# Performance work log

Measured on AMD Instinct MI355X. Metric: run time of the kernel, lower is better.

The kernel has to match this reference:

```python
import jax, jax.numpy as jnp
import numpy as np

N_SAMPLES = 32768
ATOM_LEN = 8192
N_ATOMS = 16
MODEL_DIM = 128
GRID = 128  # n_freqs == n_frames == 128
LOWEST_FREQ = 30.0 / 11025.0  # 30 Hz / nyquist of 22050 Hz


def conv2d(x, w, b, stride=1, pad=1):
    y = jax.lax.conv_general_dilated(x, w, (stride, stride), [(pad, pad), (pad, pad)],
                                     dimension_numbers=('NCHW', 'OIHW', 'NCHW'))
    return y + b[None, :, None, None]


def conv1d(x, w, b, pad=1):
    y = jax.lax.conv_general_dilated(x, w, (1,), [(pad, pad)],
                                     dimension_numbers=('NCH', 'OIH', 'NCH'))
    return y + b[None, :, None]


def lrelu(x):
    return jnp.where(x >= 0, x, 0.2 * x)


def up2d(x):
    return jnp.repeat(jnp.repeat(x, 2, axis=2), 2, axis=3)


def _forward(x, pos, wi, bi, wp, bp, ws1, bs1, ws2, bs2, ws3, bs3, ws4, bs4,
             wsb, bsb, wsel, bsel, wval, bval, wup, bup, wu1, bu1, wu2, bu2,
             wu3, bu3, wamp, bamp, wfr, bfr, wnz, bnz, noise):
    B = x.shape[0]
    h = conv2d(x, wi, bi)                                   # [B,112,128,128]
    p = jnp.broadcast_to(pos[None], (B,) + pos.shape)
    h = jnp.concatenate([h, p], axis=1)                     # [B,128,128,128]
    h = conv2d(h, wp, bp)
    # sparse trunk: /2, /2, x2, x2 back to 128x128
    h = lrelu(conv2d(h, ws1, bs1, stride=2))                # 64x64
    h = lrelu(conv2d(h, ws2, bs2, stride=2))                # 32x32
    h = up2d(h)
    h = lrelu(conv2d(h, ws3, bs3))                          # 64x64
    h = up2d(h)
    h = lrelu(conv2d(h, ws4, bs4))                          # 128x128
    # SparseBlock
    h = conv2d(h, wsb, bsb)
    norms = jnp.sqrt(jnp.sum(h * h, axis=1, keepdims=True))
    normed = h / (norms + 1e-8)
    s = conv2d(normed, wsel, bsel, pad=0)                   # [B,1,128,128]
    s = jax.nn.softmax(s.reshape(B, GRID * GRID), axis=-1)
    _, indices = jax.lax.top_k(s, N_ATOMS)                  # [B,16]
    values = conv2d(h, wval, bval, pad=0)                   # [B,128,128,128]
    f = indices // GRID
    t = indices % GRID
    # gather latents; the original multiplies by val + (1-val) == 1
    latents = values[jnp.arange(B)[:, None], :, f, t]       # [B,16,128]
    feat_map = s.reshape(B, GRID, GRID)
    # --- AudioModel on flattened atoms ---
    z = latents.reshape(B * N_ATOMS, MODEL_DIM)
    u = (z @ wup + bup).reshape(-1, MODEL_DIM, 4)           # ConvUpsample start: [N,128,4]
    for w, bb in ((wu1, bu1), (wu2, bu2), (wu3, bu3)):      # 4->8->16->32 frames
        u = jnp.repeat(u, 2, axis=2)
        u = lrelu(conv1d(u, w, bb))
    # oscillator bank: amp = params**2, freq constrained to [lowest, 1]
    amp = conv1d(u, wamp, bamp, pad=0) ** 2                 # [N,128,32]
    fr = jax.nn.sigmoid(conv1d(u, wfr, bfr, pad=0))
    fr = LOWEST_FREQ + fr * (1.0 - LOWEST_FREQ)
    amp = jnp.repeat(amp, ATOM_LEN // 32, axis=2)           # [N,128,8192]
    fr = jnp.repeat(fr, ATOM_LEN // 32, axis=2)
    phase = jnp.cumsum(fr * jnp.pi, axis=2)
    harm = jnp.sum(jnp.sin(phase) * amp, axis=1)            # [N,8192]
    # noise model: per-frame rfft magnitudes (squared) applied to white noise frames
    mags = conv1d(u, wnz, bnz, pad=0) ** 2                  # [N,129,32]
    spec = jnp.fft.rfft(noise, axis=-1)                     # [N,32,129]
    filt = spec * jnp.transpose(mags, (0, 2, 1))
    nz = jnp.fft.irfft(filt, n=256, axis=-1).reshape(-1, ATOM_LEN).astype(harm.dtype)
    atoms = (harm + nz).reshape(B, N_ATOMS, ATOM_LEN)
    # --- batched dynamic-offset scatter-add ---
    L = N_SAMPLES + ATOM_LEN
    offs = indices[:, :, None] + jnp.arange(ATOM_LEN)[None, None, :]  # [B,16,8192]
    out = jnp.zeros((B, L), atoms.dtype).at[jnp.arange(B)[:, None, None], offs].add(atoms)
    output = out[:, :N_SAMPLES][:, None, :]
    return output, latents, feat_map


def setup_inputs() -> dict:
    key = jax.random.key(0)
    ks = jax.random.split(key, 40)
    r = lambda i, shape, s=0.05: jax.random.normal(ks[i], shape, dtype=jnp.float32) * s
    B = 2
    d = {}
    d['x'] = jax.random.normal(ks[0], (B, 1, GRID, GRID), dtype=jnp.float32)
    pos = r(1, (16, GRID, GRID), 1.0)
    d['pos'] = pos / (jnp.sqrt(jnp.sum(pos * pos, axis=0, keepdims=True)) + 1e-8)
    d['wi'] = r(2, (112, 1, 3, 3)); d['bi'] = jnp.zeros(112, jnp.float32)
    d['wp'] = r(3, (128, 128, 3, 3)); d['bp'] = jnp.zeros(128, jnp.float32)
    d['ws1'] = r(4, (128, 128, 3, 3)); d['bs1'] = jnp.zeros(128, jnp.float32)
    d['ws2'] = r(5, (128, 128, 3, 3)); d['bs2'] = jnp.zeros(128, jnp.float32)
    d['ws3'] = r(6, (128, 128, 3, 3)); d['bs3'] = jnp.zeros(128, jnp.float32)
    d['ws4'] = r(7, (128, 128, 3, 3)); d['bs4'] = jnp.zeros(128, jnp.float32)
    d['wsb'] = r(8, (128, 128, 3, 3)); d['bsb'] = jnp.zeros(128, jnp.float32)
    d['wsel'] = r(9, (1, 128, 1, 1)); d['bsel'] = jnp.zeros(1, jnp.float32)
    d['wval'] = r(10, (128, 128, 1, 1)); d['bval'] = jnp.zeros(128, jnp.float32)
    d['wup'] = r(11, (128, 512)); d['bup'] = jnp.zeros(512, jnp.float32)
    d['wu1'] = r(12, (128, 128, 3)); d['bu1'] = jnp.zeros(128, jnp.float32)
    d['wu2'] = r(13, (128, 128, 3)); d['bu2'] = jnp.zeros(128, jnp.float32)
    d['wu3'] = r(14, (128, 128, 3)); d['bu3'] = jnp.zeros(128, jnp.float32)
    d['wamp'] = r(15, (128, 128, 1)); d['bamp'] = jnp.zeros(128, jnp.float32)
    d['wfr'] = r(16, (128, 128, 1)); d['bfr'] = jnp.zeros(128, jnp.float32)
    d['wnz'] = r(17, (129, 128, 1)); d['bnz'] = jnp.zeros(129, jnp.float32)
    d['noise'] = jax.random.normal(ks[18], (B * N_ATOMS, 32, 256), dtype=jnp.float32)
    return d


def reference(x, pos, wi, bi, wp, bp, ws1, bs1, ws2, bs2, ws3, bs3, ws4, bs4,
              wsb, bsb, wsel, bsel, wval, bval, wup, bup, wu1, bu1, wu2, bu2,
              wu3, bu3, wamp, bamp, wfr, bfr, wnz, bnz, noise):
    return _forward(x, pos, wi, bi, wp, bp, ws1, bs1, ws2, bs2, ws3, bs3, ws4, bs4,
                    wsb, bsb, wsel, bsel, wval, bval, wup, bup, wu1, bu1, wu2, bu2,
                    wu3, bu3, wamp, bamp, wfr, bfr, wnz, bnz, noise)
```

## Files before the change

### kernel.cpp

```cpp
#include <hip/hip_runtime.h>
#include <hip/hip_bf16.h>
#include <math.h>

#define LOWEST_FREQ (30.0f / 11025.0f)

typedef _Float16 f16x8 __attribute__((ext_vector_type(8)));
typedef _Float16 f16x4 __attribute__((ext_vector_type(4)));
typedef float f32x4 __attribute__((ext_vector_type(4)));

__device__ __forceinline__ float fast_sin_rev(float rev) {
#if __has_builtin(__builtin_amdgcn_sinf)
    return __builtin_amdgcn_sinf(rev);
#else
    return __sinf(rev * 6.28318530717958647692f);
#endif
}
__device__ __forceinline__ float fast_cos_rev(float rev) {
#if __has_builtin(__builtin_amdgcn_cosf)
    return __builtin_amdgcn_cosf(rev);
#else
    return __cosf(rev * 6.28318530717958647692f);
#endif
}
__device__ __forceinline__ float lrelu(float x) { return x >= 0.f ? x : 0.2f * x; }

__global__ __launch_bounds__(256) void repack_kernel(
    const float* __restrict__ w0, const float* __restrict__ w1,
    const float* __restrict__ w2, const float* __restrict__ w3,
    const float* __restrict__ w4, const float* __restrict__ w5,
    _Float16* __restrict__ whi, _Float16* __restrict__ wlo)
{
    int idx = blockIdx.x * 256 + threadIdx.x;
    if (idx >= 6 * 147456) return;
    int j   = idx / 147456;
    int rem = idx - j * 147456;
    int tap = rem >> 14;
    int oc  = (rem >> 7) & 127;
    int ic  = rem & 127;
    const float* src = (j == 0) ? w0 : (j == 1) ? w1 : (j == 2) ? w2 :
                       (j == 3) ? w3 : (j == 4) ? w4 : w5;
    float v = src[(oc * 128 + ic) * 9 + tap];
    _Float16 h = (_Float16)v;
    whi[idx] = h;
    wlo[idx] = (_Float16)(v - (float)h);
}

__global__ __launch_bounds__(256) void conv_in_kernel(
    const float* __restrict__ x, const float* __restrict__ wi,
    const float* __restrict__ bi, const float* __restrict__ pos,
    _Float16* __restrict__ outHi, _Float16* __restrict__ outLo, int total)
{
    int idx = blockIdx.x * 256 + threadIdx.x;
    if (idx >= total) return;
    int c   = idx & 127;
    int pix = (idx >> 7) & 16383;
    int b   = idx >> 21;
    int y = pix >> 7, xx = pix & 127;
    float v;
    if (c < 112) {
        float acc = bi[c];
        const float* xb = x + (size_t)b * 16384;
        const float* wc = wi + c * 9;
        #pragma unroll
        for (int ky = 0; ky < 3; ++ky) {
            int gy = y + ky - 1;
            if ((unsigned)gy < 128u) {
                #pragma unroll
                for (int kx = 0; kx < 3; ++kx) {
                    int gx = xx + kx - 1;
                    if ((unsigned)gx < 128u)
                        acc = fmaf(wc[ky * 3 + kx], xb[gy * 128 + gx], acc);
                }
            }
        }
        v = acc;
    } else {
        v = pos[(c - 112) * 16384 + pix];
    }
    _Float16 h = (_Float16)v;
    outHi[idx] = h;
    outLo[idx] = (_Float16)(v - (float)h);
}

template<bool UP2, bool RELU, bool SPLITOUT>
__global__ __launch_bounds__(256, 2) void mfma_conv_s1(
    const _Float16* __restrict__ inHi, const _Float16* __restrict__ inLo,
    const _Float16* __restrict__ whi, const _Float16* __restrict__ wlo,
    const float* __restrict__ bias, float* __restrict__ outF,
    _Float16* __restrict__ outHi, _Float16* __restrict__ outLo,
    int H, int W)
{
    __shared__ __align__(16) _Float16 sAh[10 * 18 * 72];
    __shared__ __align__(16) _Float16 sAl[10 * 18 * 72];
    const int tid  = threadIdx.x;
    const int w    = tid >> 6, lane = tid & 63;
    const int wm   = w & 1, wn = w >> 1;
    const int lm   = lane & 15, lq = lane >> 4;
    const int b    = blockIdx.z >> 1;
    const int ocb  = (blockIdx.z & 1) * 64;
    const int x0   = blockIdx.x * 16, y0 = blockIdx.y * 8;
    const int iy0  = y0 - 1, ix0 = x0 - 1;
    const int Hp   = UP2 ? (H >> 1) : H;
    const int Wp   = UP2 ? (W >> 1) : W;
    const _Float16* inbH = inHi + (size_t)b * Hp * Wp * 128;
    const _Float16* inbL = inLo + (size_t)b * Hp * Wp * 128;
    const f16x4 zf4 = {(_Float16)0.f, (_Float16)0.f, (_Float16)0.f, (_Float16)0.f};

    f16x4 rh[12], rl[12];

#define S1_PREF(ICS)                                                          \
    _Pragma("unroll")                                                         \
    for (int i = 0; i < 12; ++i) {                                            \
        int e = tid + i * 256;                                                \
        rh[i] = zf4; rl[i] = zf4;                                             \
        if (e < 2880) {                                                       \
            int px = e >> 4, icq = e & 15;                                    \
            int row = px / 18, col = px - row * 18;                           \
            int gy = iy0 + row, gx = ix0 + col;                               \
            if ((unsigned)gy < (unsigned)H && (unsigned)gx < (unsigned)W) {   \
                int sy = UP2 ? (gy >> 1) : gy;                                \
                int sx = UP2 ? (gx >> 1) : gx;                                \
                size_t o = ((size_t)sy * Wp + sx) * 128 + (ICS) + icq * 4;    \
                rh[i] = *(const f16x4*)(inbH + o);                            \
                rl[i] = *(const f16x4*)(inbL + o);                            \
            }                                                                 \
        }                                                                     \
    }

#define S1_WRITE()                                                            \
    _Pragma("unroll")                                                         \
    for (int i = 0; i < 12; ++i) {                                            \
        int e = tid + i * 256;                                                \
        if (e < 2880) {                                                       \
            int px = e >> 4, icq = e & 15;                                    \
            *(f16x4*)&sAh[px * 72 + icq * 4] = rh[i];                         \
            *(f16x4*)&sAl[px * 72 + icq * 4] = rl[i];                         \
        }                                                                     \
    }

    f32x4 acc[4][2];
    #pragma unroll
    for (int r = 0; r < 4; ++r)
        #pragma unroll
        for (int nt = 0; nt < 2; ++nt) acc[r][nt] = (f32x4){0.f, 0.f, 0.f, 0.f};

    S1_PREF(0)
    S1_WRITE()
    __syncthreads();

    for (int ics2 = 0; ics2 < 2; ++ics2) {
        const int ics = ics2 * 64;
        if (ics2 == 0) { S1_PREF(64) }

        for (int ky = 0; ky < 3; ++ky)
        for (int kx = 0; kx < 3; ++kx) {
            const int tap = ky * 3 + kx;
            const _Float16* wth = whi + (size_t)tap * 16384;
            const _Float16* wtl = wlo + (size_t)tap * 16384;
            #pragma unroll
            for (int kc = 0; kc < 2; ++kc) {
                f16x8 bh[2], bl[2];
                #pragma unroll
                for (int nt = 0; nt < 2; ++nt) {
                    int oc = ocb + wn * 32 + nt * 16 + lm;
                    size_t o = (size_t)oc * 128 + ics + kc * 32 + lq * 8;
                    bh[nt] = *(const f16x8*)(wth + o);
                    bl[nt] = *(const f16x8*)(wtl + o);
                }
                #pragma unroll
                for (int r = 0; r < 4; ++r) {
                    int rin = wm * 4 + r + ky;
                    int cin = lm + kx;
                    int o = (rin * 18 + cin) * 72 + kc * 32 + lq * 8;
                    f16x8 ah = *(const f16x8*)(&sAh[o]);
                    f16x8 al = *(const f16x8*)(&sAl[o]);
                    #pragma unroll
                    for (int nt = 0; nt < 2; ++nt) {
                        acc[r][nt] = __builtin_amdgcn_mfma_f32_16x16x32_f16(ah, bh[nt], acc[r][nt], 0, 0, 0);
                        acc[r][nt] = __builtin_amdgcn_mfma_f32_16x16x32_f16(ah, bl[nt], acc[r][nt], 0, 0, 0);
                        acc[r][nt] = __builtin_amdgcn_mfma_f32_16x16x32_f16(al, bh[nt], acc[r][nt], 0, 0, 0);
                    }
                }
            }
        }
        __syncthreads();
        if (ics2 == 0) { S1_WRITE() __syncthreads(); }
    }
#undef S1_PREF
#undef S1_WRITE

    float bv[2];
    #pragma unroll
    for (int nt = 0; nt < 2; ++nt) bv[nt] = bias[ocb + wn * 32 + nt * 16 + lm];
    const size_t boff = (size_t)b * H * W * 128;
    #pragma unroll
    for (int r = 0; r < 4; ++r) {
        int y = y0 + wm * 4 + r;
        #pragma unroll
        for (int nt = 0; nt < 2; ++nt) {
            int oc = ocb + wn * 32 + nt * 16 + lm;
            #pragma unroll
            for (int reg = 0; reg < 4; ++reg) {
                int xo = x0 + lq * 4 + reg;
                float vv = acc[r][nt][reg] + bv[nt];
                if (RELU) vv = lrelu(vv);
                size_t oo = boff + ((size_t)y * W + xo) * 128 + oc;
                if (SPLITOUT) {
                    _Float16 hh = (_Float16)vv;
                    outHi[oo] = hh;
                    outLo[oo] = (_Float16)(vv - (float)hh);
                } else {
                    outF[oo] = vv;
                }
            }
        }
    }
}

template<bool RELU, bool SPLITOUT>
__global__ __launch_bounds__(256, 2) void mfma_conv_s2(
    const _Float16* __restrict__ inHi, const _Float16* __restrict__ inLo,
    const _Float16* __restrict__ whi, const _Float16* __restrict__ wlo,
    const float* __restrict__ bias, float* __restrict__ outF,
    _Float16* __restrict__ outHi, _Float16* __restrict__ outLo,
    int Hin, int Win)
{
    __shared__ __align__(16) _Float16 sAh[9 * 33 * 40];
    __shared__ __align__(16) _Float16 sAl[9 * 33 * 40];
    const int tid  = threadIdx.x;
    const int w    = tid >> 6, lane = tid & 63;
    const int lm   = lane & 15, lq = lane >> 4;
    const int wn   = w;
    const int b    = blockIdx.z;
    const int Wout = Win >> 1;
    const int x0   = blockIdx.x * 16, y0 = blockIdx.y * 4;
    const int iy0  = blockIdx.y * 8 - 1, ix0 = blockIdx.x * 32 - 1;
    const _Float16* inbH = inHi + (size_t)b * Hin * Win * 128;
    const _Float16* inbL = inLo + (size_t)b * Hin * Win * 128;
    const f16x4 zf4 = {(_Float16)0.f, (_Float16)0.f, (_Float16)0.f, (_Float16)0.f};

    f16x4 rh[10], rl[10];

#define S2_PREF(ICS)                                                          \
    _Pragma("unroll")                                                         \
    for (int i = 0; i < 10; ++i) {                                            \
        int e = tid + i * 256;                                                \
        rh[i] = zf4; rl[i] = zf4;                                             \
        if (e < 2376) {                                                       \
            int px = e >> 3, icq = e & 7;                                     \
            int row = px / 33, col = px - row * 33;                           \
            int gy = iy0 + row, gx = ix0 + col;                               \
            if ((unsigned)gy < (unsigned)Hin && (unsigned)gx < (unsigned)Win) { \
                size_t o = ((size_t)gy * Win + gx) * 128 + (ICS) + icq * 4;   \
                rh[i] = *(const f16x4*)(inbH + o);                            \
                rl[i] = *(const f16x4*)(inbL + o);                            \
            }                                                                 \
        }                                                                     \
    }

#define S2_WRITE()                                                            \
    _Pragma("unroll")                                                         \
    for (int i = 0; i < 10; ++i) {                                            \
        int e = tid + i * 256;                                                \
        if (e < 2376) {                                                       \
            int px = e >> 3, icq = e & 7;                                     \
            *(f16x4*)&sAh[px * 40 + icq * 4] = rh[i];                         \
            *(f16x4*)&sAl[px * 40 + icq * 4] = rl[i];                         \
        }                                                                     \
    }

    f32x4 acc[4][2];
    #pragma unroll
    for (int r = 0; r < 4; ++r)
        #pragma unroll
        for (int nt = 0; nt < 2; ++nt) acc[r][nt] = (f32x4){0.f, 0.f, 0.f, 0.f};

    S2_PREF(0)
    S2_WRITE()
    __syncthreads();

    for (int kc = 0; kc < 4; ++kc) {
        if (kc < 3) { S2_PREF((kc + 1) * 32) }

        for (int ky = 0; ky < 3; ++ky)
        for (int kx = 0; kx < 3; ++kx) {
            const int tap = ky * 3 + kx;
            const _Float16* wth = whi + (size_t)tap * 16384;
            const _Float16* wtl = wlo + (size_t)tap * 16384;
            f16x8 bh[2], bl[2];
            #pragma unroll
            for (int nt = 0; nt < 2; ++nt) {
                int oc = wn * 32 + nt * 16 + lm;
                size_t o = (size_t)oc * 128 + kc * 32 + lq * 8;
                bh[nt] = *(const f16x8*)(wth + o);
                bl[nt] = *(const f16x8*)(wtl + o);
            }
            #pragma unroll
            for (int r = 0; r < 4; ++r) {
                int rin = 2 * r + ky;
                int cin = 2 * lm + kx;
                int o = (rin * 33 + cin) * 40 + lq * 8;
                f16x8 ah = *(const f16x8*)(&sAh[o]);
                f16x8 al = *(const f16x8*)(&sAl[o]);
                #pragma unroll
                for (int nt = 0; nt < 2; ++nt) {
                    acc[r][nt] = __builtin_amdgcn_mfma_f32_16x16x32_f16(ah, bh[nt], acc[r][nt], 0, 0, 0);
                    acc[r][nt] = __builtin_amdgcn_mfma_f32_16x16x32_f16(ah, bl[nt], acc[r][nt], 0, 0, 0);
                    acc[r][nt] = __builtin_amdgcn_mfma_f32_16x16x32_f16(al, bh[nt], acc[r][nt], 0, 0, 0);
                }
            }
        }
        __syncthreads();
        if (kc < 3) { S2_WRITE() __syncthreads(); }
    }
#undef S2_PREF
#undef S2_WRITE

    float bv[2];
    #pragma unroll
    for (int nt = 0; nt < 2; ++nt) bv[nt] = bias[wn * 32 + nt * 16 + lm];
    const int Hout = Hin >> 1;
    const size_t boff = (size_t)b * Hout * Wout * 128;
    #pragma unroll
    for (int r = 0; r < 4; ++r) {
        int y = y0 + r;
        #pragma unroll
        for (int nt = 0; nt < 2; ++nt) {
            int oc = wn * 32 + nt * 16 + lm;
            #pragma unroll
            for (int reg = 0; reg < 4; ++reg) {
                int xo = x0 + lq * 4 + reg;
                float vv = acc[r][nt][reg] + bv[nt];
                if (RELU) vv = lrelu(vv);
                size_t oo = boff + ((size_t)y * Wout + xo) * 128 + oc;
                if (SPLITOUT) {
                    _Float16 hh = (_Float16)vv;
                    outHi[oo] = hh;
                    outLo[oo] = (_Float16)(vv - (float)hh);
                } else {
                    outF[oo] = vv;
                }
            }
        }
    }
}

__global__ __launch_bounds__(256) void normsel_kernel(
    const float* __restrict__ h, const float* __restrict__ wsel,
    const float* __restrict__ bsel, float* __restrict__ s_lin, int totalPix)
{
    int wid = (blockIdx.x * 256 + threadIdx.x) >> 6;
    if (wid >= totalPix) return;
    int lane = threadIdx.x & 63;
    const float* hb = h + (size_t)wid * 128;
    float v1 = hb[lane], v2 = hb[lane + 64];
    float ss  = v1 * v1 + v2 * v2;
    float dot = wsel[lane] * v1 + wsel[lane + 64] * v2;
    #pragma unroll
    for (int off = 32; off > 0; off >>= 1) {
        ss  += __shfl_down(ss, off);
        dot += __shfl_down(dot, off);
    }
    if (lane == 0) s_lin[wid] = dot / (sqrtf(ss) + 1e-8f) + bsel[0];
}

__global__ __launch_bounds__(256) void softmax_kernel(
    const float* __restrict__ s_lin, float* __restrict__ feat)
{
    int b = blockIdx.x;
    const float* src = s_lin + b * 16384;
    __shared__ float red[256];
    int tid = threadIdx.x;
    float m = -INFINITY;
    for (int i = tid; i < 16384; i += 256) m = fmaxf(m, src[i]);
    red[tid] = m;
    __syncthreads();
    for (int off = 128; off > 0; off >>= 1) {
        if (tid < off) red[tid] = fmaxf(red[tid], red[tid + off]);
        __syncthreads();
    }
    m = red[0];
    __syncthreads();
    float s = 0.f;
    for (int i = tid; i < 16384; i += 256) s += expf(src[i] - m);
    red[tid] = s;
    __syncthreads();
    for (int off = 128; off > 0; off >>= 1) {
        if (tid < off) red[tid] += red[tid + off];
        __syncthreads();
    }
    s = red[0];
    float inv = 1.f / s;
    for (int i = tid; i < 16384; i += 256) feat[b * 16384 + i] = expf(src[i] - m) * inv;
}

__global__ __launch_bounds__(256) void topk_stage1(
    const float* __restrict__ s_lin, float* __restrict__ cand_v,
    int* __restrict__ cand_i)
{
    __shared__ float sv[256];
    int b = blockIdx.y;
    int chunk = blockIdx.x;
    int tid = threadIdx.x;
    int gidx = chunk * 256 + tid;
    float v = s_lin[b * 16384 + gidx];
    sv[tid] = v;
    __syncthreads();
    int cnt = 0;
    #pragma unroll 8
    for (int j = 0; j < 256; ++j) {
        float vj = sv[j];
        cnt += (vj > v || (vj == v && j < tid)) ? 1 : 0;
    }
    if (cnt < 16) {
        int slot = (b * 64 + chunk) * 16 + cnt;
        cand_v[slot] = v;
        cand_i[slot] = gidx;
    }
}

__global__ __launch_bounds__(1024) void topk_stage2(
    const float* __restrict__ cand_v, const int* __restrict__ cand_i,
    int* __restrict__ idxOut)
{
    __shared__ float sv[1024];
    __shared__ int   si[1024];
    int b = blockIdx.x;
    int tid = threadIdx.x;
    float v  = cand_v[b * 1024 + tid];
    int  idx = cand_i[b * 1024 + tid];
    sv[tid] = v;
    si[tid] = idx;
    __syncthreads();
    int cnt = 0;
    #pragma unroll 8
    for (int j = 0; j < 1024; ++j) {
        float vj = sv[j];
        int  ij = si[j];
        cnt += (vj > v || (vj == v && ij < idx)) ? 1 : 0;
    }
    if (cnt < 16) idxOut[b * 16 + cnt] = idx & 16383;
}

__global__ __launch_bounds__(128) void latents_kernel(
    const float* __restrict__ h, const float* __restrict__ wval,
    const float* __restrict__ bval, const int* __restrict__ tki,
    float* __restrict__ outL, float* __restrict__ zbuf)
{
    int bk = blockIdx.x;
    int oc = threadIdx.x;
    int b = bk >> 4;
    int pix = tki[bk] & 16383;
    const float* hb = h + ((size_t)b * 16384 + pix) * 128;
    const float* wr = wval + oc * 128;
    float acc = bval[oc];
    #pragma unroll 8
    for (int ic = 0; ic < 128; ++ic) acc = fmaf(wr[ic], hb[ic], acc);
    outL[bk * 128 + oc] = acc;
    zbuf[bk * 128 + oc] = acc;
}

__global__ __launch_bounds__(256) void upproj_kernel(
    const float* __restrict__ zbuf, const float* __restrict__ wup,
    const float* __restrict__ bup, float* __restrict__ u0, int total)
{
    int idx = blockIdx.x * 256 + threadIdx.x;
    if (idx >= total) return;
    int a = idx >> 9, o = idx & 511;
    const float* z = zbuf + a * 128;
    float acc = bup[o];
    #pragma unroll 8
    for (int k = 0; k < 128; ++k) acc = fmaf(z[k], wup[k * 512 + o], acc);
    u0[idx] = acc;
}

template<int LIN>
__global__ __launch_bounds__(256) void conv1dup_kernel(
    const float* __restrict__ in, const float* __restrict__ w,
    const float* __restrict__ bias, float* __restrict__ out, int total)
{
    constexpr int LOUT = 2 * LIN;
    constexpr int SH = (LIN == 4) ? 3 : (LIN == 8) ? 4 : 5;
    int idx = blockIdx.x * 256 + threadIdx.x;
    if (idx >= total) return;
    int t  = idx & (LOUT - 1);
    int oc = (idx >> SH) & 127;
    int a  = idx >> (SH + 7);
    float acc = bias[oc];
    const float* ib = in + (size_t)a * 128 * LIN;
    const float* wr = w + (size_t)oc * 384;
    int im_ = (t - 1) >> 1, i0 = t >> 1, ip = (t + 1) >> 1;
    bool bm = (t - 1) >= 0, bp = (t + 1) < LOUT;
    #pragma unroll 4
    for (int ic = 0; ic < 128; ++ic) {
        const float* ii = ib + ic * LIN;
        const float* ww = wr + ic * 3;
        if (bm) acc = fmaf(ww[0], ii[im_], acc);
        acc = fmaf(ww[1], ii[i0], acc);
        if (bp) acc = fmaf(ww[2], ii[ip], acc);
    }
    out[idx] = lrelu(acc);
}

__global__ __launch_bounds__(256) void heads_kernel(
    const float* __restrict__ u,
    const float* __restrict__ wamp, const float* __restrict__ bamp,
    const float* __restrict__ wfr,  const float* __restrict__ bfr,
    const float* __restrict__ wnz,  const float* __restrict__ bnz,
    float* __restrict__ amp, float* __restrict__ fr, float* __restrict__ mags,
    int total)
{
    int idx = blockIdx.x * 256 + threadIdx.x;
    if (idx >= total) return;
    int t  = idx & 31;
    int oc = (idx >> 5) % 385;
    int a  = idx / (32 * 385);
    const float* ib = u + (size_t)a * 4096 + t;
    const float* wr; float bv;
    if (oc < 128)      { wr = wamp + oc * 128;        bv = bamp[oc]; }
    else if (oc < 256) { wr = wfr + (oc - 128) * 128; bv = bfr[oc - 128]; }
    else               { wr = wnz + (oc - 256) * 128; bv = bnz[oc - 256]; }
    float acc = bv;
    #pragma unroll 8
    for (int ic = 0; ic < 128; ++ic) acc = fmaf(wr[ic], ib[ic * 32], acc);
    if (oc < 128) {
        amp[((size_t)a * 128 + oc) * 32 + t] = acc * acc;
    } else if (oc < 256) {
        float s = 1.f / (1.f + expf(-acc));
        fr[((size_t)a * 128 + (oc - 128)) * 32 + t] = LOWEST_FREQ + s * (1.f - LOWEST_FREQ);
    } else {
        mags[((size_t)a * 129 + (oc - 256)) * 32 + t] = acc * acc;
    }
}

__global__ __launch_bounds__(256) void prefix_kernel(
    const float* __restrict__ fr, float* __restrict__ pb, int total)
{
    int i = blockIdx.x * 256 + threadIdx.x;
    if (i >= total) return;
    const float* f = fr + i * 32;
    float* p = pb + i * 32;
    double s = 0.0;
    for (int j = 0; j < 32; ++j) {
        double t = 128.0 * s;
        p[j] = (float)(t - floor(t));
        s += (double)f[j];
    }
}

__global__ __launch_bounds__(256) void harm_kernel(
    const float* __restrict__ fr, const float* __restrict__ amp,
    const float* __restrict__ pb, const int* __restrict__ tki,
    float* __restrict__ outp, int total)
{
    int idx = blockIdx.x * 256 + threadIdx.x;
    if (idx >= total) return;
    int a = idx >> 13;
    int i = idx & 8191;
    int j = i >> 8;
    float il1 = (float)((i & 255) + 1);
    int base = a * 4096 + j;
    float acc = 0.f;
    #pragma unroll 4
    for (int c = 0; c < 128; ++c) {
        int o = base + c * 32;
        float f = fr[o];
        float am = amp[o];
        float p = pb[o];
        float rev = fmaf(il1, 0.5f * f, p);
        acc = fmaf(fast_sin_rev(rev), am, acc);
    }
    int b = a >> 4;
    atomicAdd(outp + (size_t)b * 32768 + (tki[a] & 16383) + i, acc);
}

__global__ __launch_bounds__(256) void spec_kernel(
    const float* __restrict__ noise, float* __restrict__ re,
    float* __restrict__ im, int total)
{
    int idx = blockIdx.x * 256 + threadIdx.x;
    if (idx >= total) return;
    int f  = idx % 129;
    int aw = idx / 129;
    const float* np_ = noise + (size_t)aw * 256;
    float sr = 0.f, si = 0.f;
    for (int n = 0; n < 256; ++n) {
        float rev = (float)(f * n) * (1.0f / 256.0f);
        float c = fast_cos_rev(rev);
        float s = fast_sin_rev(rev);
        float v = np_[n];
        sr = fmaf(v, c, sr);
        si = fmaf(v, -s, si);
    }
    re[idx] = sr;
    im[idx] = si;
}

__global__ __launch_bounds__(256) void nz_kernel(
    const float* __restrict__ re, const float* __restrict__ im,
    const float* __restrict__ mags, const int* __restrict__ tki,
    float* __restrict__ outp, int total)
{
    int idx = blockIdx.x * 256 + threadIdx.x;
    if (idx >= total) return;
    int t  = idx & 255;
    int w_ = (idx >> 8) & 31;
    int a  = idx >> 13;
    const float* R = re + ((size_t)a * 32 + w_) * 129;
    const float* I = im + ((size_t)a * 32 + w_) * 129;
    const float* M = mags + (size_t)a * 129 * 32 + w_;
    float acc = R[0] * M[0];
    #pragma unroll 4
    for (int f = 1; f < 128; ++f) {
        float rev = (float)(f * t) * (1.0f / 256.0f);
        float c = fast_cos_rev(rev);
        float s = fast_sin_rev(rev);
        acc = fmaf(2.f * M[f * 32], fmaf(R[f], c, -I[f] * s), acc);
    }
    float sg = (t & 1) ? -1.f : 1.f;
    acc = fmaf(M[128 * 32] * sg, R[128], acc);
    acc *= (1.f / 256.f);
    int b = a >> 4;
    atomicAdd(outp + (size_t)b * 32768 + (tki[a] & 16383) + (w_ << 8) + t, acc);
}

extern "C" void kernel_launch(void* const* d_in, const int* in_sizes, int n_in,
                              void* d_out, int out_size, void* d_ws, size_t ws_size,
                              hipStream_t stream) {
    (void)n_in; (void)ws_size;
    const float* x    = (const float*)d_in[0];
    const float* pos  = (const float*)d_in[1];
    const float* wi   = (const float*)d_in[2];
    const float* bi   = (const float*)d_in[3];
    const float* wp   = (const float*)d_in[4];
    const float* bp   = (const float*)d_in[5];
    const float* ws1  = (const float*)d_in[6];
    const float* bs1  = (const float*)d_in[7];
    const float* ws2  = (const float*)d_in[8];
    const float* bs2  = (const float*)d_in[9];
    const float* ws3  = (const float*)d_in[10];
    const float* bs3  = (const float*)d_in[11];
    const float* ws4  = (const float*)d_in[12];
    const float* bs4  = (const float*)d_in[13];
    const float* wsb  = (const float*)d_in[14];
    const float* bsb  = (const float*)d_in[15];
    const float* wsel = (const float*)d_in[16];
    const float* bsel = (const float*)d_in[17];
    const float* wval = (const float*)d_in[18];
    const float* bval = (const float*)d_in[19];
    const float* wup  = (const float*)d_in[20];
    const float* bup  = (const float*)d_in[21];
    const float* wu1  = (const float*)d_in[22];
    const float* bu1  = (const float*)d_in[23];
    const float* wu2  = (const float*)d_in[24];
    const float* bu2  = (const float*)d_in[25];
    const float* wu3  = (const float*)d_in[26];
    const float* bu3  = (const float*)d_in[27];
    const float* wamp = (const float*)d_in[28];
    const float* bamp = (const float*)d_in[29];
    const float* wfr  = (const float*)d_in[30];
    const float* bfr  = (const float*)d_in[31];
    const float* wnz  = (const float*)d_in[32];
    const float* bnz  = (const float*)d_in[33];
    const float* noise= (const float*)d_in[34];

    const int B = in_sizes[0] / (128 * 128);
    float* outp = (float*)d_out;
    float* outL = outp + (size_t)B * 32768;
    float* feat = outL + (size_t)B * 16 * 128;

    const size_t BIGF = (size_t)B * 16384 * 128;
    float* hbA = (float*)d_ws;
    float* hbB = hbA + BIGF;
    _Float16* Ahi = (_Float16*)hbA;  _Float16* Alo = Ahi + BIGF;
    _Float16* Bhi = (_Float16*)hbB;  _Float16* Blo = Bhi + BIGF;
    _Float16* whi = (_Float16*)(hbB + BIGF);
    _Float16* wlo = whi + 6 * 147456;
    float* s_lin = (float*)(wlo + 6 * 147456);
    float* tscr  = s_lin + (size_t)B * 16384;
    int*   tki   = (int*)(tscr + (size_t)B * 16384);
    float* zbuf  = (float*)(tki + 64);
    float* u0    = zbuf + (size_t)B * 2048;
    float* u1    = u0 + (size_t)B * 65536;
    float* ampb  = u1 + (size_t)B * 65536;
    float* frb   = ampb + (size_t)B * 65536;
    float* pbb   = frb + (size_t)B * 65536;
    float* magsb = pbb + (size_t)B * 65536;
    float* spR   = magsb + (size_t)B * 16 * 129 * 32;
    float* spI   = spR + (size_t)B * 16 * 32 * 129;

    float* cand_v = tscr;
    int*   cand_i = (int*)(tscr + (size_t)B * 1024);

    hipMemsetAsync(d_out, 0, (size_t)out_size * sizeof(float), stream);

    repack_kernel<<<(6 * 147456 + 255) / 256, 256, 0, stream>>>(wp, ws1, ws2, ws3, ws4, wsb, whi, wlo);

    {
        int total = B * 128 * 16384;
        conv_in_kernel<<<(total + 255) / 256, 256, 0, stream>>>(x, wi, bi, pos, Ahi, Alo, total);
    }
    mfma_conv_s1<false, false, true ><<<dim3(8, 16, B * 2), 256, 0, stream>>>(Ahi, Alo, whi + 0 * 147456, wlo + 0 * 147456, bp,  nullptr, Bhi, Blo, 128, 128);
    mfma_conv_s2<true,  true        ><<<dim3(4, 16, B),     256, 0, stream>>>(Bhi, Blo, whi + 1 * 147456, wlo + 1 * 147456, bs1, nullptr, Ahi, Alo, 128, 128);
    mfma_conv_s2<true,  true        ><<<dim3(2, 8,  B),     256, 0, stream>>>(Ahi, Alo, whi + 2 * 147456, wlo + 2 * 147456, bs2, nullptr, Bhi, Blo, 64, 64);
    mfma_conv_s1<true,  true,  true ><<<dim3(4, 8,  B * 2), 256, 0, stream>>>(Bhi, Blo, whi + 3 * 147456, wlo + 3 * 147456, bs3, nullptr, Ahi, Alo, 64, 64);
    mfma_conv_s1<true,  true,  true ><<<dim3(8, 16, B * 2), 256, 0, stream>>>(Ahi, Alo, whi + 4 * 147456, wlo + 4 * 147456, bs4, nullptr, Bhi, Blo, 128, 128);
    mfma_conv_s1<false, false, false><<<dim3(8, 16, B * 2), 256, 0, stream>>>(Bhi, Blo, whi + 5 * 147456, wlo + 5 * 147456, bsb, hbA,    nullptr, nullptr, 128, 128);
    float* h = hbA;

    {
        int totalPix = B * 16384;
        normsel_kernel<<<(totalPix * 64 + 255) / 256, 256, 0, stream>>>(h, wsel, bsel, s_lin, totalPix);
    }
    softmax_kernel<<<B, 256, 0, stream>>>(s_lin, feat);
    topk_stage1<<<dim3(64, B), 256, 0, stream>>>(s_lin, cand_v, cand_i);
    topk_stage2<<<B, 1024, 0, stream>>>(cand_v, cand_i, tki);
    latents_kernel<<<B * 16, 128, 0, stream>>>(h, wval, bval, tki, outL, zbuf);

    {
        int total = B * 16 * 512;
        upproj_kernel<<<(total + 255) / 256, 256, 0, stream>>>(zbuf, wup, bup, u0, total);
    }
    {
        int total = B * 16 * 128 * 8;
        conv1dup_kernel<4><<<(total + 255) / 256, 256, 0, stream>>>(u0, wu1, bu1, u1, total);
    }
    {
        int total = B * 16 * 128 * 16;
        conv1dup_kernel<8><<<(total + 255) / 256, 256, 0, stream>>>(u1, wu2, bu2, u0, total);
    }
    {
        int total = B * 16 * 128 * 32;
        conv1dup_kernel<16><<<(total + 255) / 256, 256, 0, stream>>>(u0, wu3, bu3, u1, total);
    }
    {
        int total = B * 16 * 385 * 32;
        heads_kernel<<<(total + 255) / 256, 256, 0, stream>>>(u1, wamp, bamp, wfr, bfr, wnz, bnz,
                                                              ampb, frb, magsb, total);
    }
    {
        int total = B * 16 * 128;
        prefix_kernel<<<(total + 255) / 256, 256, 0, stream>>>(frb, pbb, total);
    }
    {
        int total = B * 16 * 8192;
        harm_kernel<<<(total + 255) / 256, 256, 0, stream>>>(frb, ampb, pbb, tki, outp, total);
    }
    {
        int total = B * 16 * 32 * 129;
        spec_kernel<<<(total + 255) / 256, 256, 0, stream>>>(noise, spR, spI, total);
    }
    {
        int total = B * 16 * 32 * 256;
        nz_kernel<<<(total + 255) / 256, 256, 0, stream>>>(spR, spI, magsb, tki, outp, total);
    }
}
```

Before: 650.7 us.

## Fuse audio decoder stages into one kernel and parallelize softmax using topk max

```diff
diff --git a/kernel.cpp b/kernel.cpp
--- a/kernel.cpp
+++ b/kernel.cpp
@@ -364,36 +364,6 @@
     if (lane == 0) s_lin[wid] = dot / (sqrtf(ss) + 1e-8f) + bsel[0];
 }
 
-__global__ __launch_bounds__(256) void softmax_kernel(
-    const float* __restrict__ s_lin, float* __restrict__ feat)
-{
-    int b = blockIdx.x;
-    const float* src = s_lin + b * 16384;
-    __shared__ float red[256];
-    int tid = threadIdx.x;
-    float m = -INFINITY;
-    for (int i = tid; i < 16384; i += 256) m = fmaxf(m, src[i]);
-    red[tid] = m;
-    __syncthreads();
-    for (int off = 128; off > 0; off >>= 1) {
-        if (tid < off) red[tid] = fmaxf(red[tid], red[tid + off]);
-        __syncthreads();
-    }
-    m = red[0];
-    __syncthreads();
-    float s = 0.f;
-    for (int i = tid; i < 16384; i += 256) s += expf(src[i] - m);
-    red[tid] = s;
-    __syncthreads();
-    for (int off = 128; off > 0; off >>= 1) {
-        if (tid < off) red[tid] += red[tid + off];
-        __syncthreads();
-    }
-    s = red[0];
-    float inv = 1.f / s;
-    for (int i = tid; i < 16384; i += 256) feat[b * 16384 + i] = expf(src[i] - m) * inv;
-}
-
 __global__ __launch_bounds__(256) void topk_stage1(
     const float* __restrict__ s_lin, float* __restrict__ cand_v,
     int* __restrict__ cand_i)
@@ -421,7 +391,7 @@
 
 __global__ __launch_bounds__(1024) void topk_stage2(
     const float* __restrict__ cand_v, const int* __restrict__ cand_i,
-    int* __restrict__ idxOut)
+    int* __restrict__ idxOut, float* __restrict__ maxOut)
 {
     __shared__ float sv[1024];
     __shared__ int   si[1024];
@@ -439,7 +409,37 @@
         int  ij = si[j];
         cnt += (vj > v || (vj == v && ij < idx)) ? 1 : 0;
     }
-    if (cnt < 16) idxOut[b * 16 + cnt] = idx & 16383;
+    if (cnt < 16) {
+        idxOut[b * 16 + cnt] = idx & 16383;
+        if (cnt == 0) maxOut[b] = v;
+    }
+}
+
+__global__ __launch_bounds__(256) void softmax_sum_kernel(
+    const float* __restrict__ s_lin, const float* __restrict__ maxv,
+    float* __restrict__ denom)
+{
+    __shared__ float red[4];
+    int b = blockIdx.y;
+    int i = blockIdx.x * 256 + threadIdx.x;
+    float m = maxv[b];
+    float e = expf(s_lin[b * 16384 + i] - m);
+    #pragma unroll
+    for (int off = 32; off > 0; off >>= 1) e += __shfl_down(e, off);
+    int lane = threadIdx.x & 63, wv = threadIdx.x >> 6;
+    if (lane == 0) red[wv] = e;
+    __syncthreads();
+    if (threadIdx.x == 0) atomicAdd(denom + b, red[0] + red[1] + red[2] + red[3]);
+}
+
+__global__ __launch_bounds__(256) void softmax_write_kernel(
+    const float* __restrict__ s_lin, const float* __restrict__ maxv,
+    const float* __restrict__ denom, float* __restrict__ feat)
+{
+    int b = blockIdx.y;
+    int i = blockIdx.x * 256 + threadIdx.x;
+    float inv = 1.f / denom[b];
+    feat[b * 16384 + i] = expf(s_lin[b * 16384 + i] - maxv[b]) * inv;
 }
 
 __global__ __launch_bounds__(128) void latents_kernel(
@@ -460,91 +460,100 @@
     zbuf[bk * 128 + oc] = acc;
 }
 
-__global__ __launch_bounds__(256) void upproj_kernel(
-    const float* __restrict__ zbuf, const float* __restrict__ wup,
-    const float* __restrict__ bup, float* __restrict__ u0, int total)
-{
-    int idx = blockIdx.x * 256 + threadIdx.x;
-    if (idx >= total) return;
-    int a = idx >> 9, o = idx & 511;
-    const float* z = zbuf + a * 128;
-    float acc = bup[o];
-    #pragma unroll 8
-    for (int k = 0; k < 128; ++k) acc = fmaf(z[k], wup[k * 512 + o], acc);
-    u0[idx] = acc;
-}
-
 template<int LIN>
-__global__ __launch_bounds__(256) void conv1dup_kernel(
-    const float* __restrict__ in, const float* __restrict__ w,
-    const float* __restrict__ bias, float* __restrict__ out, int total)
+__device__ __forceinline__ void conv1d_stage(
+    const float* __restrict__ sIn, float* __restrict__ sOut,
+    const float* __restrict__ w, const float* __restrict__ bias, int tid)
 {
     constexpr int LOUT = 2 * LIN;
-    constexpr int SH = (LIN == 4) ? 3 : (LIN == 8) ? 4 : 5;
-    int idx = blockIdx.x * 256 + threadIdx.x;
-    if (idx >= total) return;
-    int t  = idx & (LOUT - 1);
-    int oc = (idx >> SH) & 127;
-    int a  = idx >> (SH + 7);
-    float acc = bias[oc];
-    const float* ib = in + (size_t)a * 128 * LIN;
-    const float* wr = w + (size_t)oc * 384;
-    int im_ = (t - 1) >> 1, i0 = t >> 1, ip = (t + 1) >> 1;
-    bool bm = (t - 1) >= 0, bp = (t + 1) < LOUT;
-    #pragma unroll 4
-    for (int ic = 0; ic < 128; ++ic) {
-        const float* ii = ib + ic * LIN;
-        const float* ww = wr + ic * 3;
-        if (bm) acc = fmaf(ww[0], ii[im_], acc);
-        acc = fmaf(ww[1], ii[i0], acc);
-        if (bp) acc = fmaf(ww[2], ii[ip], acc);
-    }
-    out[idx] = lrelu(acc);
-}
-
-__global__ __launch_bounds__(256) void heads_kernel(
-    const float* __restrict__ u,
+    for (int idx = tid; idx < 128 * LOUT; idx += 256) {
+        int t  = idx & (LOUT - 1);
+        int oc = idx / LOUT;
+        float acc = bias[oc];
+        const float* wr = w + (size_t)oc * 384;
+        int im_ = (t - 1) >> 1, i0 = t >> 1, ip = (t + 1) >> 1;
+        bool bm = t >= 1, bp = (t + 1) < LOUT;
+        #pragma unroll 4
+        for (int ic = 0; ic < 128; ++ic) {
+            const float* ii = sIn + ic * LIN;
+            const float* ww = wr + ic * 3;
+            if (bm) acc = fmaf(ww[0], ii[im_], acc);
+            acc = fmaf(ww[1], ii[i0], acc);
+            if (bp) acc = fmaf(ww[2], ii[ip], acc);
+        }
+        sOut[oc * LOUT + t] = lrelu(acc);
+    }
+}
+
+__global__ __launch_bounds__(256) void decoder_kernel(
+    const float* __restrict__ zbuf,
+    const float* __restrict__ wup,  const float* __restrict__ bup,
+    const float* __restrict__ wu1,  const float* __restrict__ bu1,
+    const float* __restrict__ wu2,  const float* __restrict__ bu2,
+    const float* __restrict__ wu3,  const float* __restrict__ bu3,
     const float* __restrict__ wamp, const float* __restrict__ bamp,
     const float* __restrict__ wfr,  const float* __restrict__ bfr,
     const float* __restrict__ wnz,  const float* __restrict__ bnz,
-    float* __restrict__ amp, float* __restrict__ fr, float* __restrict__ mags,
-    int total)
-{
-    int idx = blockIdx.x * 256 + threadIdx.x;
-    if (idx >= total) return;
-    int t  = idx & 31;
-    int oc = (idx >> 5) % 385;
-    int a  = idx / (32 * 385);
-    const float* ib = u + (size_t)a * 4096 + t;
-    const float* wr; float bv;
-    if (oc < 128)      { wr = wamp + oc * 128;        bv = bamp[oc]; }
-    else if (oc < 256) { wr = wfr + (oc - 128) * 128; bv = bfr[oc - 128]; }
-    else               { wr = wnz + (oc - 256) * 128; bv = bnz[oc - 256]; }
-    float acc = bv;
-    #pragma unroll 8
-    for (int ic = 0; ic < 128; ++ic) acc = fmaf(wr[ic], ib[ic * 32], acc);
-    if (oc < 128) {
-        amp[((size_t)a * 128 + oc) * 32 + t] = acc * acc;
-    } else if (oc < 256) {
-        float s = 1.f / (1.f + expf(-acc));
-        fr[((size_t)a * 128 + (oc - 128)) * 32 + t] = LOWEST_FREQ + s * (1.f - LOWEST_FREQ);
-    } else {
-        mags[((size_t)a * 129 + (oc - 256)) * 32 + t] = acc * acc;
-    }
-}
-
-__global__ __launch_bounds__(256) void prefix_kernel(
-    const float* __restrict__ fr, float* __restrict__ pb, int total)
-{
-    int i = blockIdx.x * 256 + threadIdx.x;
-    if (i >= total) return;
-    const float* f = fr + i * 32;
-    float* p = pb + i * 32;
-    double s = 0.0;
-    for (int j = 0; j < 32; ++j) {
-        double t = 128.0 * s;
-        p[j] = (float)(t - floor(t));
-        s += (double)f[j];
+    float* __restrict__ ampb, float* __restrict__ frb,
+    float* __restrict__ pbb,  float* __restrict__ magsb)
+{
+    __shared__ float sZ[128];
+    __shared__ float sA[512];
+    __shared__ float sB[1024];
+    __shared__ float sC[2048];
+    __shared__ float sD[4096];
+    __shared__ float sFr[4096];
+    const int a = blockIdx.x;
+    const int tid = threadIdx.x;
+
+    if (tid < 128) sZ[tid] = zbuf[(size_t)a * 128 + tid];
+    __syncthreads();
+
+    for (int o = tid; o < 512; o += 256) {
+        float acc = bup[o];
+        #pragma unroll 8
+        for (int k = 0; k < 128; ++k) acc = fmaf(sZ[k], wup[k * 512 + o], acc);
+        sA[o] = acc;
+    }
+    __syncthreads();
+    conv1d_stage<4>(sA, sB, wu1, bu1, tid);
+    __syncthreads();
+    conv1d_stage<8>(sB, sC, wu2, bu2, tid);
+    __syncthreads();
+    conv1d_stage<16>(sC, sD, wu3, bu3, tid);
+    __syncthreads();
+
+    for (int idx = tid; idx < 385 * 32; idx += 256) {
+        int t = idx & 31, oc = idx >> 5;
+        const float* wr; float bv;
+        if (oc < 128)      { wr = wamp + oc * 128;        bv = bamp[oc]; }
+        else if (oc < 256) { wr = wfr + (oc - 128) * 128; bv = bfr[oc - 128]; }
+        else               { wr = wnz + (oc - 256) * 128; bv = bnz[oc - 256]; }
+        float acc = bv;
+        #pragma unroll 8
+        for (int ic = 0; ic < 128; ++ic) acc = fmaf(wr[ic], sD[ic * 32 + t], acc);
+        if (oc < 128) {
+            ampb[((size_t)a * 128 + oc) * 32 + t] = acc * acc;
+        } else if (oc < 256) {
+            float s = 1.f / (1.f + expf(-acc));
+            float fv = LOWEST_FREQ + s * (1.f - LOWEST_FREQ);
+            frb[((size_t)a * 128 + (oc - 128)) * 32 + t] = fv;
+            sFr[(oc - 128) * 32 + t] = fv;
+        } else {
+            magsb[((size_t)a * 129 + (oc - 256)) * 32 + t] = acc * acc;
+        }
+    }
+    __syncthreads();
+
+    if (tid < 128) {
+        const float* f = sFr + tid * 32;
+        float* p = pbb + ((size_t)a * 128 + tid) * 32;
+        double s = 0.0;
+        for (int j = 0; j < 32; ++j) {
+            double t2 = 128.0 * s;
+            p[j] = (float)(t2 - floor(t2));
+            s += (double)f[j];
+        }
     }
 }
 
@@ -679,7 +688,9 @@
     float* s_lin = (float*)(wlo + 6 * 147456);
     float* tscr  = s_lin + (size_t)B * 16384;
     int*   tki   = (int*)(tscr + (size_t)B * 16384);
-    float* zbuf  = (float*)(tki + 64);
+    float* maxv  = (float*)(tki + 64);
+    float* denom = maxv + 16;
+    float* zbuf  = denom + 16;
     float* u0    = zbuf + (size_t)B * 2048;
     float* u1    = u0 + (size_t)B * 65536;
     float* ampb  = u1 + (size_t)B * 65536;
@@ -693,6 +704,7 @@
     int*   cand_i = (int*)(tscr + (size_t)B * 1024);
 
     hipMemsetAsync(d_out, 0, (size_t)out_size * sizeof(float), stream);
+    hipMemsetAsync(denom, 0, 16 * sizeof(float), stream);
 
     repack_kernel<<<(6 * 147456 + 255) / 256, 256, 0, stream>>>(wp, ws1, ws2, ws3, ws4, wsb, whi, wlo);
 
@@ -712,36 +724,17 @@
         int totalPix = B * 16384;
         normsel_kernel<<<(totalPix * 64 + 255) / 256, 256, 0, stream>>>(h, wsel, bsel, s_lin, totalPix);
     }
-    softmax_kernel<<<B, 256, 0, stream>>>(s_lin, feat);
     topk_stage1<<<dim3(64, B), 256, 0, stream>>>(s_lin, cand_v, cand_i);
-    topk_stage2<<<B, 1024, 0, stream>>>(cand_v, cand_i, tki);
+    topk_stage2<<<B, 1024, 0, stream>>>(cand_v, cand_i, tki, maxv);
     latents_kernel<<<B * 16, 128, 0, stream>>>(h, wval, bval, tki, outL, zbuf);
 
-    {
-        int total = B * 16 * 512;
-        upproj_kernel<<<(total + 255) / 256, 256, 0, stream>>>(zbuf, wup, bup, u0, total);
-    }
-    {
-        int total = B * 16 * 128 * 8;
-        conv1dup_kernel<4><<<(total + 255) / 256, 256, 0, stream>>>(u0, wu1, bu1, u1, total);
-    }
-    {
-        int total = B * 16 * 128 * 16;
-        conv1dup_kernel<8><<<(total + 255) / 256, 256, 0, stream>>>(u1, wu2, bu2, u0, total);
-    }
-    {
-        int total = B * 16 * 128 * 32;
-        conv1dup_kernel<16><<<(total + 255) / 256, 256, 0, stream>>>(u0, wu3, bu3, u1, total);
-    }
-    {
-        int total = B * 16 * 385 * 32;
-        heads_kernel<<<(total + 255) / 256, 256, 0, stream>>>(u1, wamp, bamp, wfr, bfr, wnz, bnz,
-                                                              ampb, frb, magsb, total);
-    }
-    {
-        int total = B * 16 * 128;
-        prefix_kernel<<<(total + 255) / 256, 256, 0, stream>>>(frb, pbb, total);
-    }
+    decoder_kernel<<<B * 16, 256, 0, stream>>>(zbuf, wup, bup, wu1, bu1, wu2, bu2, wu3, bu3,
+                                               wamp, bamp, wfr, bfr, wnz, bnz,
+                                               ampb, frb, pbb, magsb);
+
+    softmax_sum_kernel<<<dim3(64, B), 256, 0, stream>>>(s_lin, maxv, denom);
+    softmax_write_kernel<<<dim3(64, B), 256, 0, stream>>>(s_lin, maxv, denom, feat);
+
     {
         int total = B * 16 * 8192;
         harm_kernel<<<(total + 255) / 256, 256, 0, stream>>>(frb, ampb, pbb, tki, outp, total);
```

New measurement: 1.303 ms. +100.3%, slower.

## Split softmax into grid-parallel sum and write kernels, reuse top-k max

Applied to the files above, without the earlier changes.

```diff
diff --git a/kernel.cpp b/kernel.cpp
--- a/kernel.cpp
+++ b/kernel.cpp
@@ -364,36 +364,6 @@
     if (lane == 0) s_lin[wid] = dot / (sqrtf(ss) + 1e-8f) + bsel[0];
 }
 
-__global__ __launch_bounds__(256) void softmax_kernel(
-    const float* __restrict__ s_lin, float* __restrict__ feat)
-{
-    int b = blockIdx.x;
-    const float* src = s_lin + b * 16384;
-    __shared__ float red[256];
-    int tid = threadIdx.x;
-    float m = -INFINITY;
-    for (int i = tid; i < 16384; i += 256) m = fmaxf(m, src[i]);
-    red[tid] = m;
-    __syncthreads();
-    for (int off = 128; off > 0; off >>= 1) {
-        if (tid < off) red[tid] = fmaxf(red[tid], red[tid + off]);
-        __syncthreads();
-    }
-    m = red[0];
-    __syncthreads();
-    float s = 0.f;
-    for (int i = tid; i < 16384; i += 256) s += expf(src[i] - m);
-    red[tid] = s;
-    __syncthreads();
-    for (int off = 128; off > 0; off >>= 1) {
-        if (tid < off) red[tid] += red[tid + off];
-        __syncthreads();
-    }
-    s = red[0];
-    float inv = 1.f / s;
-    for (int i = tid; i < 16384; i += 256) feat[b * 16384 + i] = expf(src[i] - m) * inv;
-}
-
 __global__ __launch_bounds__(256) void topk_stage1(
     const float* __restrict__ s_lin, float* __restrict__ cand_v,
     int* __restrict__ cand_i)
@@ -421,7 +391,7 @@
 
 __global__ __launch_bounds__(1024) void topk_stage2(
     const float* __restrict__ cand_v, const int* __restrict__ cand_i,
-    int* __restrict__ idxOut)
+    int* __restrict__ idxOut, float* __restrict__ maxOut)
 {
     __shared__ float sv[1024];
     __shared__ int   si[1024];
@@ -439,7 +409,37 @@
         int  ij = si[j];
         cnt += (vj > v || (vj == v && ij < idx)) ? 1 : 0;
     }
-    if (cnt < 16) idxOut[b * 16 + cnt] = idx & 16383;
+    if (cnt < 16) {
+        idxOut[b * 16 + cnt] = idx & 16383;
+        if (cnt == 0) maxOut[b] = v;
+    }
+}
+
+__global__ __launch_bounds__(256) void softmax_sum_kernel(
+    const float* __restrict__ s_lin, const float* __restrict__ maxv,
+    float* __restrict__ denom)
+{
+    __shared__ float red[4];
+    int b = blockIdx.y;
+    int i = blockIdx.x * 256 + threadIdx.x;
+    float m = maxv[b];
+    float e = expf(s_lin[b * 16384 + i] - m);
+    #pragma unroll
+    for (int off = 32; off > 0; off >>= 1) e += __shfl_down(e, off);
+    int lane = threadIdx.x & 63, wv = threadIdx.x >> 6;
+    if (lane == 0) red[wv] = e;
+    __syncthreads();
+    if (threadIdx.x == 0) atomicAdd(denom + b, red[0] + red[1] + red[2] + red[3]);
+}
+
+__global__ __launch_bounds__(256) void softmax_write_kernel(
+    const float* __restrict__ s_lin, const float* __restrict__ maxv,
+    const float* __restrict__ denom, float* __restrict__ feat)
+{
+    int b = blockIdx.y;
+    int i = blockIdx.x * 256 + threadIdx.x;
+    float inv = 1.f / denom[b];
+    feat[b * 16384 + i] = expf(s_lin[b * 16384 + i] - maxv[b]) * inv;
 }
 
 __global__ __launch_bounds__(128) void latents_kernel(
@@ -679,7 +679,9 @@
     float* s_lin = (float*)(wlo + 6 * 147456);
     float* tscr  = s_lin + (size_t)B * 16384;
     int*   tki   = (int*)(tscr + (size_t)B * 16384);
-    float* zbuf  = (float*)(tki + 64);
+    float* maxv  = (float*)(tki + 64);
+    float* denom = maxv + 16;
+    float* zbuf  = denom + 16;
     float* u0    = zbuf + (size_t)B * 2048;
     float* u1    = u0 + (size_t)B * 65536;
     float* ampb  = u1 + (size_t)B * 65536;
@@ -693,6 +695,7 @@
     int*   cand_i = (int*)(tscr + (size_t)B * 1024);
 
     hipMemsetAsync(d_out, 0, (size_t)out_size * sizeof(float), stream);
+    hipMemsetAsync(denom, 0, 16 * sizeof(float), stream);
 
     repack_kernel<<<(6 * 147456 + 255) / 256, 256, 0, stream>>>(wp, ws1, ws2, ws3, ws4, wsb, whi, wlo);
 
@@ -712,9 +715,8 @@
         int totalPix = B * 16384;
         normsel_kernel<<<(totalPix * 64 + 255) / 256, 256, 0, stream>>>(h, wsel, bsel, s_lin, totalPix);
     }
-    softmax_kernel<<<B, 256, 0, stream>>>(s_lin, feat);
     topk_stage1<<<dim3(64, B), 256, 0, stream>>>(s_lin, cand_v, cand_i);
-    topk_stage2<<<B, 1024, 0, stream>>>(cand_v, cand_i, tki);
+    topk_stage2<<<B, 1024, 0, stream>>>(cand_v, cand_i, tki, maxv);
     latents_kernel<<<B * 16, 128, 0, stream>>>(h, wval, bval, tki, outL, zbuf);
 
     {
@@ -742,6 +744,10 @@
         int total = B * 16 * 128;
         prefix_kernel<<<(total + 255) / 256, 256, 0, stream>>>(frb, pbb, total);
     }
+
+    softmax_sum_kernel<<<dim3(64, B), 256, 0, stream>>>(s_lin, maxv, denom);
+    softmax_write_kernel<<<dim3(64, B), 256, 0, stream>>>(s_lin, maxv, denom, feat);
+
     {
         int total = B * 16 * 8192;
         harm_kernel<<<(total + 255) / 256, 256, 0, stream>>>(frb, ampb, pbb, tki, outp, total);
```

Measured after the change: 622.7 us. -4.3%, faster.
